# Kernel optimization log

Hardware: AMD Instinct MI355X
Metric: run time of the kernel (lower is better)

Reference implementation:

```python
import jax, jax.numpy as jnp
import numpy as np

D_MODEL = 1024
HEADS = 16
D_HEAD = 64  # d_q = d_k = d_v
LN_EPS = 1e-5


def setup_inputs() -> dict:
    key = jax.random.key(0)
    ks = jax.random.split(key, 12)
    B, L = 2, 2048
    query = jax.random.normal(ks[0], (B, L, D_MODEL), dtype=jnp.float32)
    k_in = jax.random.normal(ks[1], (B, L, D_MODEL), dtype=jnp.float32)
    v_in = jax.random.normal(ks[2], (B, L, D_MODEL), dtype=jnp.float32)
    # causal mask: True = masked (masked_fill with -inf); row i always keeps pos i
    mask = jnp.broadcast_to(~jnp.tril(jnp.ones((L, L), dtype=bool)), (B, L, L))
    std_qk = np.sqrt(2.0 / (D_MODEL + D_HEAD)).astype(np.float32)
    Wq = jax.random.normal(ks[3], (D_MODEL, HEADS * D_HEAD), dtype=jnp.float32) * std_qk
    Wk = jax.random.normal(ks[4], (D_MODEL, HEADS * D_HEAD), dtype=jnp.float32) * std_qk
    Wv = jax.random.normal(ks[5], (D_MODEL, HEADS * D_HEAD), dtype=jnp.float32) * std_qk
    bq = jnp.zeros((HEADS * D_HEAD,), dtype=jnp.float32)
    bk = jnp.zeros((HEADS * D_HEAD,), dtype=jnp.float32)
    bv = jnp.zeros((HEADS * D_HEAD,), dtype=jnp.float32)
    lim = 1.0 / np.sqrt(HEADS * D_HEAD)
    Wo = jax.random.uniform(ks[6], (HEADS * D_HEAD, D_MODEL), dtype=jnp.float32, minval=-lim, maxval=lim)
    bo = jax.random.uniform(ks[7], (D_MODEL,), dtype=jnp.float32, minval=-lim, maxval=lim)
    gamma = jnp.ones((D_MODEL,), dtype=jnp.float32)
    beta = jnp.zeros((D_MODEL,), dtype=jnp.float32)
    return {"query": query, "key": k_in, "value": v_in, "mask": mask,
            "Wq": Wq, "bq": bq, "Wk": Wk, "bk": bk, "Wv": Wv, "bv": bv,
            "Wo": Wo, "bo": bo, "gamma": gamma, "beta": beta}


def reference(query, key, value, mask, Wq, bq, Wk, bk, Wv, bv, Wo, bo, gamma, beta):
    B, Lq, _ = query.shape
    Lk = key.shape[1]
    # QKV projections, split into heads: [B, L, H, d]
    q = (query @ Wq + bq).reshape(B, Lq, HEADS, D_HEAD)
    k = (key @ Wk + bk).reshape(B, Lk, HEADS, D_HEAD)
    v = (value @ Wv + bv).reshape(B, Lk, HEADS, D_HEAD)
    # scaled dot-product scores: [B, H, Lq, Lk]
    scores = jnp.einsum('bqhd,bkhd->bhqk', q, k) / np.sqrt(D_HEAD).astype(np.float32)
    scores = jnp.where(mask[:, None, :, :], -jnp.inf, scores)
    probs = jax.nn.softmax(scores, axis=-1)  # dropout is identity at p=0 / eval
    out = jnp.einsum('bhqk,bkhd->bqhd', probs, v).reshape(B, Lq, HEADS * D_HEAD)
    out = out @ Wo + bo  # dropout identity
    x = query + out  # residual
    mu = jnp.mean(x, axis=-1, keepdims=True)
    var = jnp.var(x, axis=-1, keepdims=True)
    return gamma * (x - mu) * jax.lax.rsqrt(var + LN_EPS) + beta
```

## Files before the change

### kernel.cpp

```cpp
#include <hip/hip_runtime.h>
#include <hip/hip_bf16.h>

#define L_SEQ  2048
#define DMODEL 1024
#define HEADS  16
#define DHEAD  64
#define BATCH  2
#define MROWS  (BATCH * L_SEQ)

typedef __attribute__((ext_vector_type(8))) short bf16x8;
typedef __attribute__((ext_vector_type(8))) unsigned short u16x8;
typedef __attribute__((ext_vector_type(4))) float f32x4;

__device__ __forceinline__ float b2f(unsigned short u) {
    union { unsigned int u32; float f; } x;
    x.u32 = ((unsigned int)u) << 16;
    return x.f;
}
__device__ __forceinline__ unsigned short f2b(float f) {
    union { float f; unsigned int u; } x; x.f = f;
    unsigned int u = x.u;
    if ((u & 0x7fffffffu) > 0x7f800000u) return (unsigned short)((u >> 16) | 0x0040);
    unsigned int r = (u + 0x7fffu + ((u >> 16) & 1u)) >> 16;
    return (unsigned short)r;
}
__device__ __forceinline__ unsigned short f2br(float f) {
    union { float f; unsigned int u; } x; x.f = f;
    return (unsigned short)((x.u + 0x7fffu + ((x.u >> 16) & 1u)) >> 16);
}

__device__ __forceinline__ float4 load4(const void* p, int isF32, size_t idx) {
    if (isF32) return *(const float4*)((const float*)p + idx);
    const ushort4 u = *(const ushort4*)((const unsigned short*)p + idx);
    return make_float4(b2f(u.x), b2f(u.y), b2f(u.z), b2f(u.w));
}
__device__ __forceinline__ float load1(const void* p, int isF32, size_t idx) {
    return isF32 ? ((const float*)p)[idx] : b2f(((const unsigned short*)p)[idx]);
}

__device__ __forceinline__ void gload16(const void* g, void* l) {
    __builtin_amdgcn_global_load_lds(
        (const __attribute__((address_space(1))) void*)g,
        (__attribute__((address_space(3))) void*)l, 16, 0, 0);
}

__global__ void detect_kernel(const unsigned short* __restrict__ q, int* __restrict__ flag) {
    int cnt = 0;
    #pragma unroll 8
    for (int t = 0; t < 64; ++t) {
        const unsigned short u = q[(threadIdx.x << 6) + t];
        const int e = (u >> 7) & 0xFF;
        cnt += (e >= 133) ? 1 : 0;
    }
    #pragma unroll
    for (int off = 32; off; off >>= 1) cnt += __shfl_xor(cnt, off);
    if (threadIdx.x == 0) *flag = (cnt > 64) ? 1 : 0;
}

__global__ void diag_kernel(float* __restrict__ out, float val, int n) {
    const int i = blockIdx.x * 256 + threadIdx.x;
    if (i < n) out[i] = val;
}

__global__ __launch_bounds__(256) void cvtW_kernel(
    const void* __restrict__ W0, const void* __restrict__ W1,
    const void* __restrict__ W2, const void* __restrict__ W3,
    unsigned short* __restrict__ T0, unsigned short* __restrict__ T1,
    unsigned short* __restrict__ T2, unsigned short* __restrict__ T3,
    const int* __restrict__ dflag)
{
    const int isF32 = *dflag;
    const int z = blockIdx.z;
    const void* W = (z == 0) ? W0 : (z == 1) ? W1 : (z == 2) ? W2 : W3;
    unsigned short* T = (z == 0) ? T0 : (z == 1) ? T1 : (z == 2) ? T2 : T3;

    __shared__ unsigned short tile[64][66];
    const int kb = blockIdx.x << 6, nb = blockIdx.y << 6;
    const int tr = threadIdx.x >> 4, tc = (threadIdx.x & 15) << 2;
    #pragma unroll
    for (int p = 0; p < 4; ++p) {
        const int r = tr + p * 16;
        const float4 v = load4(W, isF32, (size_t)(kb + r) * DMODEL + nb + tc);
        tile[tc + 0][r] = f2br(v.x);
        tile[tc + 1][r] = f2br(v.y);
        tile[tc + 2][r] = f2br(v.z);
        tile[tc + 3][r] = f2br(v.w);
    }
    __syncthreads();
    #pragma unroll
    for (int p = 0; p < 4; ++p) {
        const int rr = tr + p * 16;
        const ushort4 o = make_ushort4(tile[rr][tc], tile[rr][tc + 1],
                                       tile[rr][tc + 2], tile[rr][tc + 3]);
        *(ushort4*)(T + (size_t)(nb + rr) * DMODEL + kb + tc) = o;
    }
}

#define QSTAGE_B(BP, K0)                                                          \
    _Pragma("unroll")                                                             \
    for (int s = 0; s < 2; ++s)                                                   \
        gload16(Wt + (size_t)(colBase + (wid << 5) + (s << 4) + (lane >> 2)) * DMODEL \
                    + (K0) + qsw,                                                 \
                (BP) + ((wid << 5) + (s << 4)) * 32);

#define QSTAGE_A_BF16(BP, K0)                                                     \
    gload16((const unsigned short*)A + (size_t)(rowBase + (wid << 4) + (lane >> 2)) * DMODEL \
                    + (K0) + qsw,                                                 \
            (BP) + (wid << 4) * 32);

#define QCOMPUTE(AP, BP)                                                          \
    {                                                                             \
        bf16x8 af[4], bfr[4];                                                     \
        _Pragma("unroll")                                                         \
        for (int i = 0; i < 4; ++i) {                                             \
            const int row = wm + i * 16 + ln;                                     \
            af[i] = *(const bf16x8*)((AP) + row * 32 + ((quad ^ (row & 3)) << 3)); \
        }                                                                         \
        _Pragma("unroll")                                                         \
        for (int j = 0; j < 4; ++j) {                                             \
            const int rowb = wn + j * 16 + ln;                                    \
            bfr[j] = *(const bf16x8*)((BP) + rowb * 32 + ((quad ^ (rowb & 3)) << 3)); \
        }                                                                         \
        _Pragma("unroll")                                                         \
        for (int i = 0; i < 4; ++i)                                               \
            _Pragma("unroll")                                                     \
            for (int j = 0; j < 4; ++j)                                           \
                acc[i][j] = __builtin_amdgcn_mfma_f32_16x16x32_bf16(              \
                    af[i], bfr[j], acc[i][j], 0, 0, 0);                           \
    }

#define QPACK_A(PK, X0, X1)                                                       \
    PK[0] = f2br(X0.x); PK[1] = f2br(X0.y); PK[2] = f2br(X0.z); PK[3] = f2br(X0.w); \
    PK[4] = f2br(X1.x); PK[5] = f2br(X1.y); PK[6] = f2br(X1.z); PK[7] = f2br(X1.w);

__global__ __launch_bounds__(512) void gemm_qkv_mfma(
    const void* __restrict__ A0, const void* __restrict__ A1, const void* __restrict__ A2,
    const unsigned short* __restrict__ Wt0, const unsigned short* __restrict__ Wt1,
    const unsigned short* __restrict__ Wt2,
    const void* __restrict__ b0, const void* __restrict__ b1, const void* __restrict__ b2,
    unsigned short* __restrict__ O0, unsigned short* __restrict__ O1, unsigned short* __restrict__ O2,
    const int* __restrict__ dflag)
{
    const int isF32 = *dflag;

    const int bid = blockIdx.x;
    const int xcd = bid & 7;
    const int jj  = bid >> 3;
    const int g   = xcd * 48 + jj;
    const int z   = g >> 7;
    const int rem = g & 127;
    const int rowBase = (rem >> 2) << 7;
    const int colBase = (rem & 3) << 8;

    const void* A  = (z == 0) ? A0 : (z == 1) ? A1 : A2;
    const unsigned short* Wt = (z == 0) ? Wt0 : (z == 1) ? Wt1 : Wt2;
    const void* bi = (z == 0) ? b0 : (z == 1) ? b1 : b2;
    unsigned short* out = (z == 0) ? O0 : (z == 1) ? O1 : O2;
    const float scale = (z == 0) ? 0.125f : 1.0f;

    __shared__ __align__(16) unsigned short As[2][128 * 32];
    __shared__ __align__(16) unsigned short Bs[2][256 * 32];

    const int tid  = threadIdx.x;
    const int lane = tid & 63, wid = tid >> 6;
    const int ln   = lane & 15, quad = lane >> 4;
    const int wm   = (wid & 1) << 6;
    const int wn   = (wid >> 1) << 6;
    const int qsw  = (((lane & 3) ^ ((lane >> 2) & 3)) << 3);

    f32x4 acc[4][4];
    #pragma unroll
    for (int i = 0; i < 4; ++i)
        #pragma unroll
        for (int j = 0; j < 4; ++j)
            #pragma unroll
            for (int d = 0; d < 4; ++d) acc[i][j][d] = 0.f;

    if (isF32) {
        const int am = tid >> 2, kseg = tid & 3;
        const int ac = (kseg ^ (am & 3)) << 3;
        const size_t abase = (size_t)(rowBase + am) * DMODEL + (kseg << 3);

        QSTAGE_B(Bs[0], 0)
        {
            const float4 a0 = load4(A, 1, abase);
            const float4 a1 = load4(A, 1, abase + 4);
            u16x8 pk;
            QPACK_A(pk, a0, a1)
            *(u16x8*)(As[0] + am * 32 + ac) = pk;
        }
        __syncthreads();

        int cur = 0;
        for (int t = 0; t < 31; ++t) {
            const int nxt = cur ^ 1;
            const int k0n = (t + 1) << 5;
            QSTAGE_B(Bs[nxt], k0n)
            const float4 a0 = load4(A, 1, abase + k0n);
            const float4 a1 = load4(A, 1, abase + k0n + 4);

            QCOMPUTE(As[cur], Bs[cur])

            u16x8 pk;
            QPACK_A(pk, a0, a1)
            *(u16x8*)(As[nxt] + am * 32 + ac) = pk;

            __syncthreads();
            cur = nxt;
        }
        QCOMPUTE(As[cur], Bs[cur])
    } else {
        QSTAGE_B(Bs[0], 0)
        QSTAGE_A_BF16(As[0], 0)
        __syncthreads();
        int cur = 0;
        for (int t = 0; t < 31; ++t) {
            const int nxt = cur ^ 1;
            const int k0n = (t + 1) << 5;
            QSTAGE_B(Bs[nxt], k0n)
            QSTAGE_A_BF16(As[nxt], k0n)
            QCOMPUTE(As[cur], Bs[cur])
            __syncthreads();
            cur = nxt;
        }
        QCOMPUTE(As[cur], Bs[cur])
    }

    float bsv[4];
    #pragma unroll
    for (int j = 0; j < 4; ++j) bsv[j] = load1(bi, isF32, colBase + wn + j * 16 + ln);

    if (z != 2) {
        #pragma unroll
        for (int i = 0; i < 4; ++i) {
            const int r0 = rowBase + wm + i * 16 + quad * 4;
            const int b = r0 >> 11, l0 = r0 & (L_SEQ - 1);
            #pragma unroll
            for (int j = 0; j < 4; ++j) {
                const int n = colBase + wn + j * 16 + ln;
                const int h = n >> 6, d = n & 63;
                const size_t base = ((size_t)(b * HEADS + h) * L_SEQ) << 6;
                #pragma unroll
                for (int reg = 0; reg < 4; ++reg)
                    out[base + ((size_t)(l0 + reg) << 6) + d] =
                        f2br((acc[i][j][reg] + bsv[j]) * scale);
            }
        }
    } else {
        #pragma unroll
        for (int i = 0; i < 4; ++i) {
            const int r0 = rowBase + wm + i * 16 + quad * 4;
            const int b = r0 >> 11, l0 = r0 & (L_SEQ - 1);
            #pragma unroll
            for (int j = 0; j < 4; ++j) {
                const int n = colBase + wn + j * 16 + ln;
                const int h = n >> 6, d = n & 63;
                ushort4 o;
                o.x = f2br(acc[i][j][0] + bsv[j]);
                o.y = f2br(acc[i][j][1] + bsv[j]);
                o.z = f2br(acc[i][j][2] + bsv[j]);
                o.w = f2br(acc[i][j][3] + bsv[j]);
                *(ushort4*)(out + (((size_t)((b * HEADS + h) * 64 + d)) << 11) + l0) = o;
            }
        }
    }
}

#define STAGE_B64(BP, K0)                                                         \
    _Pragma("unroll")                                                             \
    for (int s = 0; s < 4; ++s)                                                   \
        gload16(Wt + (size_t)(colBase + (wid << 5) + (s << 3) + brow8) * DMODEL + (K0) + bswz, \
                (BP) + ((wid << 5) + (s << 3)) * 64);

#define STAGE_A64(AP, BASE, K0)                                                   \
    _Pragma("unroll")                                                             \
    for (int s = 0; s < 2; ++s)                                                   \
        gload16((BASE) + (size_t)(rowBase + (wid << 4) + (s << 3) + brow8) * DMODEL + (K0) + bswz, \
                (AP) + ((wid << 4) + (s << 3)) * 64);

#define GEMM_COMPUTE64(AP, BP)                                                    \
    {                                                                             \
        bf16x8 af[2][2], bfr[4][2];                                               \
        _Pragma("unroll")                                                         \
        for (int i = 0; i < 2; ++i) {                                             \
            const int row = wm + i * 16 + ln;                                     \
            _Pragma("unroll")                                                     \
            for (int kc = 0; kc < 2; ++kc)                                        \
                af[i][kc] = *(const bf16x8*)((AP) + row * 64 +                    \
                            ((((kc << 2) | quad) ^ (ln & 7)) << 3));              \
        }                                                                         \
        _Pragma("unroll")                                                         \
        for (int j = 0; j < 4; ++j) {                                             \
            const int rowb = wn + j * 16 + ln;                                    \
            _Pragma("unroll")                                                     \
            for (int kc = 0; kc < 2; ++kc)                                        \
                bfr[j][kc] = *(const bf16x8*)((BP) + rowb * 64 +                  \
                            ((((kc << 2) | quad) ^ (ln & 7)) << 3));              \
        }                                                                         \
        _Pragma("unroll")                                                         \
        for (int kc = 0; kc < 2; ++kc)                                            \
            _Pragma("unroll")                                                     \
            for (int i = 0; i < 2; ++i)                                           \
                _Pragma("unroll")                                                 \
                for (int j = 0; j < 4; ++j)                                       \
                    acc[i][j] = __builtin_amdgcn_mfma_f32_16x16x32_bf16(          \
                        af[i][kc], bfr[j][kc], acc[i][j], 0, 0, 0);               \
    }

__global__ __launch_bounds__(256) void gemm_out_mfma(
    const unsigned short* __restrict__ AO,
    const unsigned short* __restrict__ Wt,
    const void* __restrict__ bi,
    const void* __restrict__ resid,
    float* __restrict__ X,
    const int* __restrict__ dflag)
{
    const int isF32 = *dflag;
    __shared__ __align__(16) unsigned short As[2][64 * 64];
    __shared__ __align__(16) unsigned short Bs[2][128 * 64];

    const int bid = blockIdx.x;
    const int xcd = bid & 7;
    const int jj  = bid >> 3;
    const int g   = xcd * 8 + (jj >> 3);
    const int rowBase = g << 6;
    const int colBase = (jj & 7) << 7;

    const int tid  = threadIdx.x;
    const int lane = tid & 63, wid = tid >> 6;
    const int ln   = lane & 15, quad = lane >> 4;
    const int wm   = (wid & 1) << 5;
    const int wn   = (wid >> 1) << 6;

    f32x4 acc[2][4];
    #pragma unroll
    for (int i = 0; i < 2; ++i)
        #pragma unroll
        for (int j = 0; j < 4; ++j)
            #pragma unroll
            for (int d = 0; d < 4; ++d) acc[i][j][d] = 0.f;

    const int brow8 = lane >> 3;
    const int bswz  = ((lane & 7) ^ ((lane >> 3) & 7)) << 3;

    STAGE_B64(Bs[0], 0)
    STAGE_A64(As[0], AO, 0)
    __syncthreads();

    int cur = 0;
    for (int t = 0; t < 15; ++t) {
        const int nxt = cur ^ 1;
        const int k0n = (t + 1) << 6;
        STAGE_B64(Bs[nxt], k0n)
        STAGE_A64(As[nxt], AO, k0n)
        GEMM_COMPUTE64(As[cur], Bs[cur])
        __syncthreads();
        cur = nxt;
    }
    GEMM_COMPUTE64(As[cur], Bs[cur])

    float bsv[4];
    #pragma unroll
    for (int j = 0; j < 4; ++j) bsv[j] = load1(bi, isF32, colBase + wn + j * 16 + ln);

    #pragma unroll
    for (int i = 0; i < 2; ++i) {
        const int r0 = rowBase + wm + i * 16 + quad * 4;
        #pragma unroll
        for (int j = 0; j < 4; ++j) {
            const int n = colBase + wn + j * 16 + ln;
            #pragma unroll
            for (int reg = 0; reg < 4; ++reg) {
                const size_t idx = (size_t)(r0 + reg) * DMODEL + n;
                X[idx] = acc[i][j][reg] + bsv[j] + load1(resid, isF32, idx);
            }
        }
    }
}

#define KVB  128
#define NQB  (L_SEQ / 64)
#define KSTR 72
#define VSTR 136
__global__ __launch_bounds__(256, 3) void attn_mfma_kernel(
    const unsigned short* __restrict__ Q,
    const unsigned short* __restrict__ K,
    const unsigned short* __restrict__ Vt,
    unsigned short* __restrict__ AO)
{
    __shared__ unsigned short Kl[KVB * KSTR];
    __shared__ unsigned short Vl[64 * VSTR];
    __shared__ unsigned short Pl[4][16 * KVB];

    const int tid  = threadIdx.x;
    const int wid  = tid >> 6;
    const int lane = tid & 63;
    const int ln   = lane & 15;
    const int quad = lane >> 4;

    const int xcd = blockIdx.x & 7;
    const int jj  = blockIdx.x >> 3;
    const int bh  = xcd * 4 + (jj & 3);
    const int qb  = (NQB - 1) - (jj >> 2);

    const size_t qkBase = (size_t)bh * (L_SEQ * 64);
    const size_t vtBase = (size_t)bh * (64 * L_SEQ);

    const int qrow = qb * 64 + wid * 16 + ln;
    const bf16x8 qf0 = *(const bf16x8*)(Q + qkBase + (size_t)qrow * 64 + quad * 8);
    const bf16x8 qf1 = *(const bf16x8*)(Q + qkBase + (size_t)qrow * 64 + quad * 8 + 32);

    f32x4 o[4];
    #pragma unroll
    for (int d = 0; d < 4; ++d) { o[d][0] = 0.f; o[d][1] = 0.f; o[d][2] = 0.f; o[d][3] = 0.f; }
    float m[4] = {-INFINITY, -INFINITY, -INFINITY, -INFINITY};
    float l[4] = {0.f, 0.f, 0.f, 0.f};

    unsigned short* Pw = Pl[wid];
    const int kp_r = tid >> 3, kp_c = (tid & 7) * 8;
    const int vp_r = tid >> 4, vp_c = (tid & 15) * 8;

    const int nt = (qb >> 1) + 1;
    for (int jt = 0; jt < nt; ++jt) {
        __syncthreads();
        #pragma unroll
        for (int p = 0; p < 4; ++p) {
            const int kr = kp_r + p * 32;
            *(int4*)(Kl + kr * KSTR + kp_c) =
                *(const int4*)(K + qkBase + (size_t)(jt * KVB + kr) * 64 + kp_c);
            const int vr = vp_r + p * 16;
            *(int4*)(Vl + vr * VSTR + vp_c) =
                *(const int4*)(Vt + vtBase + (size_t)vr * L_SEQ + jt * KVB + vp_c);
        }
        __syncthreads();

        f32x4 s[8];
        __builtin_amdgcn_s_setprio(1);
        #pragma unroll
        for (int sub = 0; sub < 8; ++sub) {
            const bf16x8 kf0 = *(const bf16x8*)(Kl + (sub * 16 + ln) * KSTR + quad * 8);
            const bf16x8 kf1 = *(const bf16x8*)(Kl + (sub * 16 + ln) * KSTR + quad * 8 + 32);
            f32x4 a2;
            a2[0] = 0.f; a2[1] = 0.f; a2[2] = 0.f; a2[3] = 0.f;
            a2 = __builtin_amdgcn_mfma_f32_16x16x32_bf16(qf0, kf0, a2, 0, 0, 0);
            a2 = __builtin_amdgcn_mfma_f32_16x16x32_bf16(qf1, kf1, a2, 0, 0, 0);
            s[sub] = a2;
        }
        __builtin_amdgcn_s_setprio(0);

        if (jt == nt - 1) {
            const int row0 = qb * 64 + wid * 16 + quad * 4;
            #pragma unroll
            for (int sub = 0; sub < 8; ++sub) {
                const int keyg = jt * KVB + sub * 16 + ln;
                #pragma unroll
                for (int reg = 0; reg < 4; ++reg)
                    if (keyg > row0 + reg) s[sub][reg] = -INFINITY;
            }
        }

        float alpha[4];
        #pragma unroll
        for (int reg = 0; reg < 4; ++reg) {
            float t = fmaxf(
                fmaxf(fmaxf(s[0][reg], s[1][reg]), fmaxf(s[2][reg], s[3][reg])),
                fmaxf(fmaxf(s[4][reg], s[5][reg]), fmaxf(s[6][reg], s[7][reg])));
            #pragma unroll
            for (int off = 8; off; off >>= 1) t = fmaxf(t, __shfl_xor(t, off));
            const float mn = fmaxf(m[reg], t);
            alpha[reg] = __expf(m[reg] - mn);
            m[reg] = mn;
            float rs = 0.f;
            #pragma unroll
            for (int sub = 0; sub < 8; ++sub) {
                const float pe = __expf(s[sub][reg] - mn);
                s[sub][reg] = pe;
                rs += pe;
            }
            #pragma unroll
            for (int off = 8; off; off >>= 1) rs += __shfl_xor(rs, off);
            l[reg] = l[reg] * alpha[reg] + rs;
        }

        #pragma unroll
        for (int sub = 0; sub < 8; ++sub)
            #pragma unroll
            for (int reg = 0; reg < 4; ++reg) {
                const int r = quad * 4 + reg;
                const int blk = (sub * 2 + (ln >> 3)) ^ ((r >> 1) & 7);
                Pw[r * KVB + blk * 8 + (ln & 7)] = f2br(s[sub][reg]);
            }

        #pragma unroll
        for (int dblk = 0; dblk < 4; ++dblk)
            #pragma unroll
            for (int reg = 0; reg < 4; ++reg)
                o[dblk][reg] *= alpha[reg];

        __builtin_amdgcn_s_setprio(1);
        #pragma unroll
        for (int jb = 0; jb < 4; ++jb) {
            const int rblk = (jb * 4 + quad) ^ ((ln >> 1) & 7);
            const bf16x8 pf = *(const bf16x8*)(Pw + ln * KVB + rblk * 8);
            #pragma unroll
            for (int dblk = 0; dblk < 4; ++dblk) {
                const bf16x8 vf = *(const bf16x8*)(Vl + (dblk * 16 + ln) * VSTR + jb * 32 + quad * 8);
                o[dblk] = __builtin_amdgcn_mfma_f32_16x16x32_bf16(pf, vf, o[dblk], 0, 0, 0);
            }
        }
        __builtin_amdgcn_s_setprio(0);
    }

    const int b = bh >> 4, h = bh & 15;
    float rl[4];
    #pragma unroll
    for (int reg = 0; reg < 4; ++reg) rl[reg] = 1.f / l[reg];
    #pragma unroll
    for (int dblk = 0; dblk < 4; ++dblk)
        #pragma unroll
        for (int reg = 0; reg < 4; ++reg) {
            const int row = qb * 64 + wid * 16 + quad * 4 + reg;
            AO[((size_t)(b * L_SEQ + row)) * DMODEL + h * 64 + dblk * 16 + ln] =
                f2b(o[dblk][reg] * rl[reg]);
        }
}

__global__ __launch_bounds__(256) void ln_kernel(
    const float* __restrict__ X,
    const void* __restrict__ gamma,
    const void* __restrict__ beta,
    float* __restrict__ out,
    const int* __restrict__ dflag)
{
    const int isF32 = *dflag;
    const int row = blockIdx.x;
    const int tid = threadIdx.x;
    const float* x = X + (size_t)row * DMODEL;
    const int c0 = tid << 2;
    const float4 vv = *(const float4*)(x + c0);
    float s  = vv.x + vv.y + vv.z + vv.w;
    float s2 = vv.x * vv.x + vv.y * vv.y + vv.z * vv.z + vv.w * vv.w;
    #pragma unroll
    for (int off = 32; off; off >>= 1) {
        s  += __shfl_xor(s, off);
        s2 += __shfl_xor(s2, off);
    }
    __shared__ float red[4][2];
    const int wid = tid >> 6, lane = tid & 63;
    if (lane == 0) { red[wid][0] = s; red[wid][1] = s2; }
    __syncthreads();
    s  = red[0][0] + red[1][0] + red[2][0] + red[3][0];
    s2 = red[0][1] + red[1][1] + red[2][1] + red[3][1];
    const float mu  = s * (1.f / 1024.f);
    const float var = s2 * (1.f / 1024.f) - mu * mu;
    const float inv = rsqrtf(var + 1e-5f);
    const float4 gm = load4(gamma, isF32, c0);
    const float4 bt = load4(beta,  isF32, c0);
    float4 r;
    r.x = gm.x * (vv.x - mu) * inv + bt.x;
    r.y = gm.y * (vv.y - mu) * inv + bt.y;
    r.z = gm.z * (vv.z - mu) * inv + bt.z;
    r.w = gm.w * (vv.w - mu) * inv + bt.w;
    if (!(r.x == r.x) || fabsf(r.x) > 1e37f) r.x = 777000.0f;
    if (!(r.y == r.y) || fabsf(r.y) > 1e37f) r.y = 777000.0f;
    if (!(r.z == r.z) || fabsf(r.z) > 1e37f) r.z = 777000.0f;
    if (!(r.w == r.w) || fabsf(r.w) > 1e37f) r.w = 777000.0f;
    *(float4*)(out + (size_t)row * DMODEL + c0) = r;
}

extern "C" void kernel_launch(void* const* d_in, const int* in_sizes, int n_in,
                              void* d_out, int out_size, void* d_ws, size_t ws_size,
                              hipStream_t stream) {
    const void* query = d_in[0];
    const void* key   = d_in[1];
    const void* value = d_in[2];

    int wbase = 4;
    if (in_sizes[3] == DMODEL * DMODEL) wbase = 3;
    const void* Wq    = d_in[wbase + 0];
    const void* bq    = d_in[wbase + 1];
    const void* Wk    = d_in[wbase + 2];
    const void* bk    = d_in[wbase + 3];
    const void* Wv    = d_in[wbase + 4];
    const void* bv    = d_in[wbase + 5];
    const void* Wo    = d_in[wbase + 6];
    const void* bo    = d_in[wbase + 7];
    const void* gamma = d_in[wbase + 8];
    const void* beta  = d_in[wbase + 9];

    const size_t NEED = ((size_t)24u << 20) + 64;
    if (ws_size < NEED) {
        const float val = (float)(ws_size >> 20) * 1000.0f;
        diag_kernel<<<dim3((out_size + 255) / 256), dim3(256), 0, stream>>>(
            (float*)d_out, val, out_size);
        return;
    }

    char* ws = (char*)d_ws;
    unsigned short* Qb  = (unsigned short*)(ws);
    unsigned short* Kb  = (unsigned short*)(ws + (size_t)( 8u << 20));
    unsigned short* Vtb = (unsigned short*)(ws + (size_t)(16u << 20));
    float* X            = (float*)ws;
    int* dflag          = (int*)(ws + (size_t)(24u << 20));
    unsigned short* AO  = (unsigned short*)d_out;
    unsigned short* Wtq = (unsigned short*)d_out + ((size_t)4u << 20);
    unsigned short* Wtk = Wtq + ((size_t)1u << 20);
    unsigned short* Wtv = Wtk + ((size_t)1u << 20);
    unsigned short* Wto = Wtv + ((size_t)1u << 20);

    const dim3 blk(256);

    detect_kernel<<<dim3(1), dim3(64), 0, stream>>>((const unsigned short*)query, dflag);
    cvtW_kernel<<<dim3(16, 16, 4), blk, 0, stream>>>(
        Wq, Wk, Wv, Wo, Wtq, Wtk, Wtv, Wto, dflag);
    gemm_qkv_mfma<<<dim3(384), dim3(512), 0, stream>>>(
        query, key, value, Wtq, Wtk, Wtv, bq, bk, bv, Qb, Kb, Vtb, dflag);
    attn_mfma_kernel<<<dim3(BATCH * HEADS * 32), blk, 0, stream>>>(Qb, Kb, Vtb, AO);
    gemm_out_mfma<<<dim3(512), blk, 0, stream>>>(AO, Wto, bo, query, X, dflag);
    ln_kernel<<<dim3(MROWS), blk, 0, stream>>>(X, gamma, beta, (float*)d_out, dflag);
}
```

Before: 277.6 us.

## Use direct-to-LDS loads with XOR swizzle in attention and lazy softmax rescale

The attention kernel now stages K and V tiles with direct global-to-LDS 16-byte loads into unpadded, XOR-swizzled shared buffers instead of register round-trip copies into padded arrays. The online softmax skips the max update and rescaling of the output and row sum when the new tile max exceeds the running max by at most 8 across the whole wavefront. The QKV GEMM swizzle pattern also changes to use row>>1. These aim to cut LDS staging cost and VALU work, but skipping the rescale lets unnormalised exponentials reach up to e^8, which risks bf16 precision loss in P.

```diff
diff --git a/kernel.cpp b/kernel.cpp
--- a/kernel.cpp
+++ b/kernel.cpp
@@ -114,12 +114,12 @@
         _Pragma("unroll")                                                         \
         for (int i = 0; i < 4; ++i) {                                             \
             const int row = wm + i * 16 + ln;                                     \
-            af[i] = *(const bf16x8*)((AP) + row * 32 + ((quad ^ (row & 3)) << 3)); \
+            af[i] = *(const bf16x8*)((AP) + row * 32 + ((quad ^ ((row >> 1) & 3)) << 3)); \
         }                                                                         \
         _Pragma("unroll")                                                         \
         for (int j = 0; j < 4; ++j) {                                             \
             const int rowb = wn + j * 16 + ln;                                    \
-            bfr[j] = *(const bf16x8*)((BP) + rowb * 32 + ((quad ^ (rowb & 3)) << 3)); \
+            bfr[j] = *(const bf16x8*)((BP) + rowb * 32 + ((quad ^ ((rowb >> 1) & 3)) << 3)); \
         }                                                                         \
         _Pragma("unroll")                                                         \
         for (int i = 0; i < 4; ++i)                                               \
@@ -166,7 +166,7 @@
     const int ln   = lane & 15, quad = lane >> 4;
     const int wm   = (wid & 1) << 6;
     const int wn   = (wid >> 1) << 6;
-    const int qsw  = (((lane & 3) ^ ((lane >> 2) & 3)) << 3);
+    const int qsw  = (((lane & 3) ^ ((lane >> 3) & 3)) << 3);
 
     f32x4 acc[4][4];
     #pragma unroll
@@ -178,7 +178,7 @@
 
     if (isF32) {
         const int am = tid >> 2, kseg = tid & 3;
-        const int ac = (kseg ^ (am & 3)) << 3;
+        const int ac = (kseg ^ ((am >> 1) & 3)) << 3;
         const size_t abase = (size_t)(rowBase + am) * DMODEL + (kseg << 3);
 
         QSTAGE_B(Bs[0], 0)
@@ -380,16 +380,33 @@
 
 #define KVB  128
 #define NQB  (L_SEQ / 64)
-#define KSTR 72
-#define VSTR 136
+
+#define KSTAGE(JT)                                                                \
+    _Pragma("unroll")                                                             \
+    for (int s = 0; s < 4; ++s) {                                                 \
+        const int r0 = (wid << 5) + (s << 3);                                     \
+        gload16(K + qkBase + (size_t)((JT) * KVB + r0 + (lane >> 3)) * 64         \
+                    + (((lane & 7) ^ (lane >> 3)) << 3),                          \
+                Kl + r0 * 64);                                                    \
+    }
+#define VSTAGE(JT)                                                                \
+    _Pragma("unroll")                                                             \
+    for (int s = 0; s < 4; ++s) {                                                 \
+        const int r0 = (wid << 4) + (s << 2);                                     \
+        const int vr = r0 + (lane >> 4);                                          \
+        gload16(Vt + vtBase + (size_t)vr * L_SEQ + (JT) * KVB                     \
+                    + (((lane & 15) ^ (vr & 15)) << 3),                           \
+                Vl + r0 * 128);                                                   \
+    }
+
 __global__ __launch_bounds__(256, 3) void attn_mfma_kernel(
     const unsigned short* __restrict__ Q,
     const unsigned short* __restrict__ K,
     const unsigned short* __restrict__ Vt,
     unsigned short* __restrict__ AO)
 {
-    __shared__ unsigned short Kl[KVB * KSTR];
-    __shared__ unsigned short Vl[64 * VSTR];
+    __shared__ __align__(16) unsigned short Kl[KVB * 64];
+    __shared__ __align__(16) unsigned short Vl[64 * KVB];
     __shared__ unsigned short Pl[4][16 * KVB];
 
     const int tid  = threadIdx.x;
@@ -417,29 +434,21 @@
     float l[4] = {0.f, 0.f, 0.f, 0.f};
 
     unsigned short* Pw = Pl[wid];
-    const int kp_r = tid >> 3, kp_c = (tid & 7) * 8;
-    const int vp_r = tid >> 4, vp_c = (tid & 15) * 8;
 
     const int nt = (qb >> 1) + 1;
     for (int jt = 0; jt < nt; ++jt) {
         __syncthreads();
-        #pragma unroll
-        for (int p = 0; p < 4; ++p) {
-            const int kr = kp_r + p * 32;
-            *(int4*)(Kl + kr * KSTR + kp_c) =
-                *(const int4*)(K + qkBase + (size_t)(jt * KVB + kr) * 64 + kp_c);
-            const int vr = vp_r + p * 16;
-            *(int4*)(Vl + vr * VSTR + vp_c) =
-                *(const int4*)(Vt + vtBase + (size_t)vr * L_SEQ + jt * KVB + vp_c);
-        }
+        KSTAGE(jt)
+        VSTAGE(jt)
         __syncthreads();
 
         f32x4 s[8];
         __builtin_amdgcn_s_setprio(1);
         #pragma unroll
         for (int sub = 0; sub < 8; ++sub) {
-            const bf16x8 kf0 = *(const bf16x8*)(Kl + (sub * 16 + ln) * KSTR + quad * 8);
-            const bf16x8 kf1 = *(const bf16x8*)(Kl + (sub * 16 + ln) * KSTR + quad * 8 + 32);
+            const int krow = sub * 16 + ln;
+            const bf16x8 kf0 = *(const bf16x8*)(Kl + krow * 64 + ((quad ^ (ln & 7)) << 3));
+            const bf16x8 kf1 = *(const bf16x8*)(Kl + krow * 64 + (((quad + 4) ^ (ln & 7)) << 3));
             f32x4 a2;
             a2[0] = 0.f; a2[1] = 0.f; a2[2] = 0.f; a2[3] = 0.f;
             a2 = __builtin_amdgcn_mfma_f32_16x16x32_bf16(qf0, kf0, a2, 0, 0, 0);
@@ -459,7 +468,8 @@
             }
         }
 
-        float alpha[4];
+        float t4[4];
+        float need = -1e30f;
         #pragma unroll
         for (int reg = 0; reg < 4; ++reg) {
             float t = fmaxf(
@@ -467,19 +477,32 @@
                 fmaxf(fmaxf(s[4][reg], s[5][reg]), fmaxf(s[6][reg], s[7][reg])));
             #pragma unroll
             for (int off = 8; off; off >>= 1) t = fmaxf(t, __shfl_xor(t, off));
-            const float mn = fmaxf(m[reg], t);
-            alpha[reg] = __expf(m[reg] - mn);
-            m[reg] = mn;
+            t4[reg] = t;
+            need = fmaxf(need, t - m[reg]);
+        }
+        const bool skip = __all(need <= 8.0f) != 0;
+
+        float alpha[4];
+        if (!skip) {
+            #pragma unroll
+            for (int reg = 0; reg < 4; ++reg) {
+                const float mn = fmaxf(m[reg], t4[reg]);
+                alpha[reg] = __expf(m[reg] - mn);
+                m[reg] = mn;
+            }
+        }
+        #pragma unroll
+        for (int reg = 0; reg < 4; ++reg) {
             float rs = 0.f;
             #pragma unroll
             for (int sub = 0; sub < 8; ++sub) {
-                const float pe = __expf(s[sub][reg] - mn);
+                const float pe = __expf(s[sub][reg] - m[reg]);
                 s[sub][reg] = pe;
                 rs += pe;
             }
             #pragma unroll
             for (int off = 8; off; off >>= 1) rs += __shfl_xor(rs, off);
-            l[reg] = l[reg] * alpha[reg] + rs;
+            l[reg] = skip ? (l[reg] + rs) : (l[reg] * alpha[reg] + rs);
         }
 
         #pragma unroll
@@ -491,11 +514,13 @@
                 Pw[r * KVB + blk * 8 + (ln & 7)] = f2br(s[sub][reg]);
             }
 
-        #pragma unroll
-        for (int dblk = 0; dblk < 4; ++dblk)
-            #pragma unroll
-            for (int reg = 0; reg < 4; ++reg)
-                o[dblk][reg] *= alpha[reg];
+        if (!skip) {
+            #pragma unroll
+            for (int dblk = 0; dblk < 4; ++dblk)
+                #pragma unroll
+                for (int reg = 0; reg < 4; ++reg)
+                    o[dblk][reg] *= alpha[reg];
+        }
 
         __builtin_amdgcn_s_setprio(1);
         #pragma unroll
@@ -504,7 +529,9 @@
             const bf16x8 pf = *(const bf16x8*)(Pw + ln * KVB + rblk * 8);
             #pragma unroll
             for (int dblk = 0; dblk < 4; ++dblk) {
-                const bf16x8 vf = *(const bf16x8*)(Vl + (dblk * 16 + ln) * VSTR + jb * 32 + quad * 8);
+                const int vrow = dblk * 16 + ln;
+                const bf16x8 vf = *(const bf16x8*)(Vl + vrow * 128 +
+                                                   (((jb * 4 + quad) ^ ln) << 3));
                 o[dblk] = __builtin_amdgcn_mfma_f32_16x16x32_bf16(pf, vf, o[dblk], 0, 0, 0);
             }
         }
```

Result: no change. 274.8 us (-1.0%).
